# Kernel tuning notes

Hardware: AMD Instinct MI355X
Metric: run time of the kernel (lower is better)

The kernel has to match this reference:

```python
import jax, jax.numpy as jnp
import numpy as np

B, C = 2, 8
SPATIAL = (128, 128, 128)


def setup_inputs() -> dict:
    key = jax.random.key(0)
    k1, k2 = jax.random.split(key)
    pred = jax.random.normal(k1, (B, C) + SPATIAL, dtype=jnp.float32)
    ref = jax.random.randint(k2, (B, 1) + SPATIAL, 0, C, dtype=jnp.int32)
    return {"pred": pred, "ref": ref}


def reference(pred, ref):
    # Hard Dice, exclude_background=True (background index 0), weighted=False,
    # labels = range(nb_class), reduction='mean'.
    b, c = pred.shape[0], pred.shape[1]
    pred_lbl = jnp.argmax(pred, axis=1).reshape(b, -1)   # (B, S) int labels
    ref_lbl = ref.reshape(b, -1)                          # (B, S) int labels

    classes = jnp.arange(1, c, dtype=pred_lbl.dtype)      # skip background (index 0)
    # (B, C-1, S) boolean one-vs-all masks; single pass over the volume per tensor.
    p1 = pred_lbl[:, None, :] == classes[None, :, None]
    r1 = ref_lbl[:, None, :] == classes[None, :, None]

    inter = jnp.sum(p1 & r1, axis=-1).astype(jnp.float32)  # (B, C-1)
    psum = jnp.sum(p1, axis=-1).astype(jnp.float32)
    rsum = jnp.sum(r1, axis=-1).astype(jnp.float32)

    hasref = rsum > 0                                      # (B, C-1)
    union = psum + rsum
    # torch: loss1 = 2*inter/union then masked_fill_(~hasref, 0)
    dice = jnp.where(hasref, 2.0 * inter / jnp.where(union > 0, union, 1.0), 0.0)

    sumweights = jnp.sum(hasref.astype(jnp.float32), axis=1)  # (B,)
    loss = jnp.sum(dice, axis=1) / sumweights                 # (B,)
    return jnp.mean(loss)                                     # reduction='mean'
```

## Files before the change

kernel.cpp:

```cpp
#include <hip/hip_runtime.h>


#define S_VOX (128 * 128 * 128)
#define S4    (S_VOX / 4)
#define NC    8
#define NFG   7
#define NT    262144
#define NITER (S4 / NT)

#define WS_INTS (2 * 3 * NFG)

#define PROC_COMP(C)                                                     \
    {                                                                    \
        float bv = a0.C; int bi = 0;                                     \
        if (a1.C > bv) { bv = a1.C; bi = 1; }                            \
        if (a2.C > bv) { bv = a2.C; bi = 2; }                            \
        if (a3.C > bv) { bv = a3.C; bi = 3; }                            \
        if (a4.C > bv) { bv = a4.C; bi = 4; }                            \
        if (a5.C > bv) { bv = a5.C; bi = 5; }                            \
        if (a6.C > bv) { bv = a6.C; bi = 6; }                            \
        if (a7.C > bv) { bv = a7.C; bi = 7; }                            \
        const int rr = r.C;                                              \
        _Pragma("unroll")                                                \
        for (int c = 1; c < NC; ++c) {                                   \
            const unsigned long long mp = __ballot(bi == c);             \
            const unsigned long long mr = __ballot(rr == c);             \
            cp[c - 1] += (int)__popcll(mp);                              \
            cr[c - 1] += (int)__popcll(mr);                              \
            ci[c - 1] += (int)__popcll(mp & mr);                         \
        }                                                                \
    }

__global__ __launch_bounds__(256) void dice_count_kernel(
    const float4* __restrict__ pred4, const int4* __restrict__ ref4,
    int* __restrict__ ws)
{
    const int b = blockIdx.y;
    int ci[NFG], cp[NFG], cr[NFG];
#pragma unroll
    for (int k = 0; k < NFG; ++k) { ci[k] = 0; cp[k] = 0; cr[k] = 0; }

    const int tid = blockIdx.x * 256 + threadIdx.x;
    const long long predBase = (long long)b * NC * S4;
    const long long refBase  = (long long)b * S4;

#pragma unroll
    for (int it = 0; it < NITER; ++it) {
        const int g = tid + it * NT;
        const float4 a0 = pred4[predBase + (long long)0 * S4 + g];
        const float4 a1 = pred4[predBase + (long long)1 * S4 + g];
        const float4 a2 = pred4[predBase + (long long)2 * S4 + g];
        const float4 a3 = pred4[predBase + (long long)3 * S4 + g];
        const float4 a4 = pred4[predBase + (long long)4 * S4 + g];
        const float4 a5 = pred4[predBase + (long long)5 * S4 + g];
        const float4 a6 = pred4[predBase + (long long)6 * S4 + g];
        const float4 a7 = pred4[predBase + (long long)7 * S4 + g];
        const int4   r  = ref4[refBase + g];
        PROC_COMP(x)
        PROC_COMP(y)
        PROC_COMP(z)
        PROC_COMP(w)
    }

    __shared__ int sh[3 * NFG];
    if (threadIdx.x < 3 * NFG) sh[threadIdx.x] = 0;
    __syncthreads();

    const int lane = threadIdx.x & 63;
    if (lane == 0) {
#pragma unroll
        for (int k = 0; k < NFG; ++k) {
            atomicAdd(&sh[k], ci[k]);
            atomicAdd(&sh[NFG + k], cp[k]);
            atomicAdd(&sh[2 * NFG + k], cr[k]);
        }
    }
    __syncthreads();

    if (threadIdx.x < 3 * NFG) {
        atomicAdd(&ws[b * (3 * NFG) + threadIdx.x], sh[threadIdx.x]);
    }
}

__global__ void dice_finalize_kernel(const int* __restrict__ ws,
                                     float* __restrict__ out)
{
    if (blockIdx.x == 0 && threadIdx.x == 0) {
        float total = 0.0f;
#pragma unroll
        for (int b = 0; b < 2; ++b) {
            const int* w = ws + b * (3 * NFG);
            float sumd = 0.0f, sumw = 0.0f;
#pragma unroll
            for (int k = 0; k < NFG; ++k) {
                const int I = w[k];
                const int P = w[NFG + k];
                const int R = w[2 * NFG + k];
                if (R > 0) {
                    sumw += 1.0f;
                    sumd += 2.0f * (float)I / (float)(P + R);
                }
            }
            total += sumd / sumw;
        }
        out[0] = 0.5f * total;
    }
}

extern "C" void kernel_launch(void* const* d_in, const int* in_sizes, int n_in,
                              void* d_out, int out_size, void* d_ws, size_t ws_size,
                              hipStream_t stream) {
    const float* pred = (const float*)d_in[0];
    const int*   ref  = (const int*)d_in[1];
    float*       out  = (float*)d_out;
    int*         ws   = (int*)d_ws;

    hipMemsetAsync(ws, 0, WS_INTS * sizeof(int), stream);

    dim3 grid(1024, 2, 1);
    dim3 block(256, 1, 1);
    dice_count_kernel<<<grid, block, 0, stream>>>(
        (const float4*)pred, (const int4*)ref, ws);
    dice_finalize_kernel<<<1, 64, 0, stream>>>(ws, out);
}
```

Baseline: 217.2 us.

## Replace global atomics and memset with per-block partials, shrink grid

Each block now writes its 21 counters into its own workspace slot instead of doing global atomicAdds, and the finalize kernel reduces the 512 slots in parallel before computing the dice. This drops the hipMemsetAsync launch and the atomic contention on one small region. The grid shrinks from 1024 to 256 blocks per batch, so each thread runs more iterations, with partial unroll by 2 to limit register pressure. Fewer blocks may cut occupancy or memory parallelism on a purely bandwidth-bound streaming kernel.

```diff
diff --git a/kernel.cpp b/kernel.cpp
--- a/kernel.cpp
+++ b/kernel.cpp
@@ -5,10 +5,13 @@
 #define S4    (S_VOX / 4)
 #define NC    8
 #define NFG   7
-#define NT    262144
+#define NCNT  (3 * NFG)
+
+#define GX    256
+#define NT    (GX * 256)
 #define NITER (S4 / NT)
 
-#define WS_INTS (2 * 3 * NFG)
+#define NSLOT (2 * GX)
 
 #define PROC_COMP(C)                                                     \
     {                                                                    \
@@ -44,7 +47,7 @@
     const long long predBase = (long long)b * NC * S4;
     const long long refBase  = (long long)b * S4;
 
-#pragma unroll
+#pragma unroll 2
     for (int it = 0; it < NITER; ++it) {
         const int g = tid + it * NT;
         const float4 a0 = pred4[predBase + (long long)0 * S4 + g];
@@ -62,12 +65,11 @@
         PROC_COMP(w)
     }
 
-    __shared__ int sh[3 * NFG];
-    if (threadIdx.x < 3 * NFG) sh[threadIdx.x] = 0;
+    __shared__ int sh[NCNT];
+    if (threadIdx.x < NCNT) sh[threadIdx.x] = 0;
     __syncthreads();
 
-    const int lane = threadIdx.x & 63;
-    if (lane == 0) {
+    if ((threadIdx.x & 63) == 0) {
 #pragma unroll
         for (int k = 0; k < NFG; ++k) {
             atomicAdd(&sh[k], ci[k]);
@@ -77,19 +79,33 @@
     }
     __syncthreads();
 
-    if (threadIdx.x < 3 * NFG) {
-        atomicAdd(&ws[b * (3 * NFG) + threadIdx.x], sh[threadIdx.x]);
+    const int slot = b * GX + blockIdx.x;
+    if (threadIdx.x < NCNT) {
+        ws[threadIdx.x * NSLOT + slot] = sh[threadIdx.x];
     }
 }
 
 __global__ void dice_finalize_kernel(const int* __restrict__ ws,
                                      float* __restrict__ out)
 {
-    if (blockIdx.x == 0 && threadIdx.x == 0) {
+    __shared__ int tot[2 * NCNT];
+    const int t = threadIdx.x;
+    if (t < 2 * NCNT) {
+        const int b2 = t / NCNT;
+        const int jj = t % NCNT;
+        const int* base = ws + jj * NSLOT + b2 * GX;
+        int s = 0;
+#pragma unroll 8
+        for (int i = 0; i < GX; ++i) s += base[i];
+        tot[t] = s;
+    }
+    __syncthreads();
+
+    if (t == 0) {
         float total = 0.0f;
 #pragma unroll
-        for (int b = 0; b < 2; ++b) {
-            const int* w = ws + b * (3 * NFG);
+        for (int b2 = 0; b2 < 2; ++b2) {
+            const int* w = tot + b2 * NCNT;
             float sumd = 0.0f, sumw = 0.0f;
 #pragma unroll
             for (int k = 0; k < NFG; ++k) {
@@ -115,9 +131,7 @@
     float*       out  = (float*)d_out;
     int*         ws   = (int*)d_ws;
 
-    hipMemsetAsync(ws, 0, WS_INTS * sizeof(int), stream);
-
-    dim3 grid(1024, 2, 1);
+    dim3 grid(GX, 2, 1);
     dim3 block(256, 1, 1);
     dice_count_kernel<<<grid, block, 0, stream>>>(
         (const float4*)pred, (const int4*)ref, ws);
```

Result: faster. 211.1 us (-2.8%).
